# Optimization experiments

Measured on AMD Instinct MI355X. Metric: run time of the kernel, lower is better.

The kernel has to match this reference:

```python
import jax, jax.numpy as jnp
import numpy as np

D_MODEL = 1024
H = 4
DK = 128   # head_qk_dim (key_dim=512)
DV = 256   # head_v_dim (value_dim=1024)
EPS = 1e-5
SCALE = DK ** -0.5


def setup_inputs() -> dict:
    key = jax.random.key(0)
    ks = jax.random.split(key, 8)
    w = lambda k, i, o: jax.random.normal(k, (i, o), jnp.float32) * (2.0 ** -2.5) * (6.0 / (i + o)) ** 0.5 * 2
    return {
        "x": jax.random.normal(ks[0], (2, 4096, D_MODEL), jnp.float32),
        "Wq": w(ks[1], D_MODEL, H * DK),
        "Wk": w(ks[2], D_MODEL, H * DK),
        "Wv": w(ks[3], D_MODEL, H * DV),
        "Wb": w(ks[4], D_MODEL, H),
        "Wg": w(ks[5], D_MODEL, H * DV),
        "Wo": w(ks[6], H * DV, D_MODEL),
        "norm_w": jnp.ones((DV,), jnp.float32),
    }


def _delta_rule(q, k, v, beta):
    """Delta-rule linear attention. q,k: [b,n,h,dk], v: [b,n,h,dv], beta: [b,n,h].
    S_t = S_{t-1} + k_t (beta_t * (v_t - k_t^T S_{t-1}))^T ; o_t = q_t^T S_t."""
    b = q.shape[0]
    # time-major for scan: [n,b,h,*]
    qt = jnp.moveaxis(q, 1, 0)
    kt = jnp.moveaxis(k, 1, 0)
    vt = jnp.moveaxis(v, 1, 0)
    bt = jnp.moveaxis(beta, 1, 0)
    S0 = jnp.zeros((b, H, DK, DV), q.dtype)

    def step(S, inp):
        q_t, k_t, v_t, b_t = inp
        pred = jnp.einsum('bhk,bhkv->bhv', k_t, S)          # current memory readout
        delta = (v_t - pred) * b_t[..., None]                # beta-scaled error
        S = S + k_t[..., :, None] * delta[..., None, :]      # rank-1 update [b,h,dk,dv]
        o_t = jnp.einsum('bhk,bhkv->bhv', q_t, S)
        return S, o_t

    _, o = jax.lax.scan(step, S0, (qt, kt, vt, bt))          # o: [n,b,h,dv]
    return jnp.moveaxis(o, 0, 1)                             # [b,n,h,dv]


def reference(x, Wq, Wk, Wv, Wb, Wg, Wo, norm_w):
    b, n, _ = x.shape
    q = (x @ Wq).reshape(b, n, H, DK)
    k = (x @ Wk).reshape(b, n, H, DK)
    v = (x @ Wv).reshape(b, n, H, DV)
    beta = jax.nn.sigmoid(x @ Wb)                            # [b,n,h]
    # L2-normalize keys (delta-rule kernels assume unit-norm k) and scale q
    k = k * jax.lax.rsqrt(jnp.sum(k * k, axis=-1, keepdims=True) + 1e-12)
    q = q * SCALE
    o = _delta_rule(q, k, v, beta)                           # [b,n,h,dv]
    # FusedRMSNormSwishGate over head_v_dim
    g = (x @ Wg).reshape(b, n, H, DV)
    o = o * jax.lax.rsqrt(jnp.mean(o * o, axis=-1, keepdims=True) + EPS) * norm_w
    o = o * (g * jax.nn.sigmoid(g))                          # swish gate
    return o.reshape(b, n, H * DV) @ Wo
```

## Files before the change

kernel.cpp:

```cpp
#include <hip/hip_runtime.h>
#include <hip/hip_bf16.h>
#include <stdint.h>
#include <stddef.h>

typedef __attribute__((ext_vector_type(8))) short short8v;
typedef __attribute__((ext_vector_type(4))) float f32x4;
typedef unsigned short us;

__device__ __forceinline__ float bf2f(unsigned short u) {
    return __uint_as_float(((unsigned int)u) << 16);
}
__device__ __forceinline__ unsigned short f2bf(float f) {
    unsigned int x = __float_as_uint(f);
    x += 0x7fffu + ((x >> 16) & 1u);
    return (unsigned short)(x >> 16);
}
__device__ __forceinline__ unsigned int cvtpk(float lo, float hi) {
    unsigned int r;
    asm("v_cvt_pk_bf16_f32 %0, %1, %2" : "=v"(r) : "v"(lo), "v"(hi));
    return r;
}

#define NTOK 8192
#define DM   1024
#define NPROJ 3072
#define SEQ  4096
#define NCHUNK 64
#define SCQ 0.08838834764831845f

#define GLDS16(g, l) __builtin_amdgcn_global_load_lds( \
    (const __attribute__((address_space(1))) void*)(g), \
    (__attribute__((address_space(3))) void*)(l), 16, 0, 0)

__device__ __forceinline__ void bar_lgkm() {
    asm volatile("s_waitcnt lgkmcnt(0)" ::: "memory");
    __builtin_amdgcn_s_barrier();
    __builtin_amdgcn_sched_barrier(0);
}

__device__ __forceinline__ int sw16(int row, int k) {
    int u = k >> 3;
    int us_ = (u & 8) | ((u ^ row) & 7);
    return row * 128 + us_ * 8 + (k & 7);
}
__device__ __forceinline__ int sw8(int row, int k) {
    int u = k >> 3;
    int us_ = (u ^ row) & 7;
    return row * 64 + us_ * 8 + (k & 7);
}
__device__ __forceinline__ int sw128(int row, int k) {
    int u = k >> 3;
    return row * 128 + ((u ^ row) & 15) * 8 + (k & 7);
}
__device__ __forceinline__ int sw64(int row, int k) {
    int u = k >> 3;
    return row * 64 + ((u ^ row) & 7) * 8 + (k & 7);
}
__device__ __forceinline__ int sw64b(int row, int k) {
    int u = k >> 3;
    return row * 64 + ((u ^ row ^ (row >> 3)) & 7) * 8 + (k & 7);
}
__device__ __forceinline__ int swU(int t, int j) {
    int jj = j & 127, u = jj >> 3;
    int us_ = (u & 8) | ((u ^ t) & 7);
    return t * 256 + (j >> 7) * 128 + us_ * 8 + (jj & 7);
}

__global__ __launch_bounds__(256) void prep(
    const float* __restrict__ x, us* __restrict__ xb,
    const float* __restrict__ Wb, float* __restrict__ beta,
    const float* __restrict__ Wq, const float* __restrict__ Wk,
    const float* __restrict__ Wv, const float* __restrict__ Wg,
    const float* __restrict__ Wo, us* __restrict__ WT, us* __restrict__ WoT)
{
    __shared__ float smem[64 * 65];
    int tid = threadIdx.x;
    int bid = blockIdx.x;

    if (bid < 4096) {
        int i = bid * 256 + tid;
        int tok = i >> 7;
        int kb = (i >> 3) & 15;
        int u = i & 7;
        int ko = kb * 64 + ((u ^ (tok & 7)) * 8);
        const float4* src = (const float4*)(x + (size_t)tok * 1024 + ko);
        float4 v0 = src[0], v1 = src[1];
        uint4 o;
        o.x = cvtpk(v0.x, v0.y); o.y = cvtpk(v0.z, v0.w);
        o.z = cvtpk(v1.x, v1.y); o.w = cvtpk(v1.z, v1.w);
        *(uint4*)(xb + (size_t)i * 8) = o;
        const float4* wbv = (const float4*)Wb;
        float xs[8] = {v0.x, v0.y, v0.z, v0.w, v1.x, v1.y, v1.z, v1.w};
        float4 s = {0.f, 0.f, 0.f, 0.f};
        #pragma unroll
        for (int e = 0; e < 8; e++) {
            float4 w = wbv[ko + e];
            s.x += xs[e] * w.x; s.y += xs[e] * w.y;
            s.z += xs[e] * w.z; s.w += xs[e] * w.w;
        }
        *(float4*)&smem[tid * 4] = s;
        __syncthreads();
        if (tid < 8) {
            int tp = tid >> 2, h = tid & 3;
            float acc = 0.f;
            for (int j = 0; j < 128; j++) acc += smem[(tp * 128 + j) * 4 + h];
            beta[(size_t)(bid * 2 + tp) * 4 + h] = 1.f / (1.f + __expf(-acc));
        }
        return;
    }

    int lb = bid - 4096;
    const float* srcw; us* dst; int N;
    if (lb < 128)      { srcw = Wq; dst = WT;                    N = 512;  }
    else if (lb < 256) { srcw = Wk; dst = WT + (size_t)512 * DM;  N = 512;  lb -= 128; }
    else if (lb < 512) { srcw = Wv; dst = WT + (size_t)1024 * DM; N = 1024; lb -= 256; }
    else if (lb < 768) { srcw = Wg; dst = WT + (size_t)2048 * DM; N = 1024; lb -= 512; }
    else               { srcw = Wo; dst = WoT;                   N = 1024; lb -= 768; }
    int nbx = N >> 6;
    int n0 = (lb % nbx) * 64, k0 = (lb / nbx) * 64;
    float (*tl)[65] = (float(*)[65])smem;
    int tr = tid >> 6, tc = tid & 63;
    #pragma unroll
    for (int i2 = 0; i2 < 16; i2++) {
        int kk = 4 * i2 + tr;
        tl[kk][tc] = srcw[(size_t)(k0 + kk) * N + n0 + tc];
    }
    __syncthreads();
    int n = tid >> 2, seg = (tid & 3) * 16;
    short8v a, b;
    #pragma unroll
    for (int e = 0; e < 8; e++) {
        a[e] = (short)f2bf(tl[seg + e][n]);
        b[e] = (short)f2bf(tl[seg + 8 + e][n]);
    }
    int n_ = n0 + n;
    int o1 = (tid & 3) * 2, o2_ = o1 + 1;
    us* d = dst + (size_t)n_ * DM + k0;
    *(short8v*)(d + (o1 ^ (n_ & 7)) * 8) = a;
    *(short8v*)(d + (o2_ ^ (n_ & 7)) * 8) = b;
}

template<int OUT_F32>
__global__ __launch_bounds__(256) void gemm_bt(
    const us* __restrict__ A, const us* __restrict__ BT,
    void* __restrict__ C, int M, int N, int K)
{
    __shared__ us As[2][128 * 64];
    __shared__ us Bs[2][128 * 64];
    int tid = threadIdx.x;
    int wave = tid >> 6, lane = tid & 63;
    int wr = (wave >> 1) * 64, wc = (wave & 1) * 64;
    int fr = lane & 15, fq = lane >> 4;
    int nbx = gridDim.x, nwg = nbx * gridDim.y;
    int wg = blockIdx.y * nbx + blockIdx.x;
    int cpx = nwg >> 3;
    wg = (wg & 7) * cpx + (wg >> 3);
    int m0 = (wg % nbx) * 128, n0 = (wg / nbx) * 128;

    f32x4 acc[4][4];
    #pragma unroll
    for (int i = 0; i < 4; i++)
        #pragma unroll
        for (int j = 0; j < 4; j++) acc[i][j] = (f32x4){0.f, 0.f, 0.f, 0.f};

    int rl = lane >> 3, ul = lane & 7;

    auto issue = [&](int k0, int bufi) {
        #pragma unroll
        for (int i = 0; i < 4; i++) {
            int row = wave * 32 + i * 8 + rl;
            GLDS16(&A[(size_t)(m0 + row) * K + k0 + ul * 8], &As[bufi][(wave * 32 + i * 8) * 64]);
            GLDS16(&BT[(size_t)(n0 + row) * K + k0 + ul * 8], &Bs[bufi][(wave * 32 + i * 8) * 64]);
        }
    };

    int NT = K >> 6;
    issue(0, 0);
    if (NT > 1) issue(64, 1);

    for (int t = 0; t < NT; t++) {
        if (t + 1 < NT) asm volatile("s_waitcnt vmcnt(8)" ::: "memory");
        else            asm volatile("s_waitcnt vmcnt(0)" ::: "memory");
        __builtin_amdgcn_sched_barrier(0);
        __builtin_amdgcn_s_barrier();
        __builtin_amdgcn_sched_barrier(0);
        const us* as = As[t & 1];
        const us* bs = Bs[t & 1];
        #pragma unroll
        for (int kk = 0; kk < 2; kk++) {
            short8v a[4], b[4];
            #pragma unroll
            for (int i = 0; i < 4; i++) {
                int ra = wr + i * 16 + fr;
                a[i] = *(const short8v*)&as[ra * 64 + ((4 * kk + fq) ^ (ra & 7)) * 8];
                int rb = wc + i * 16 + fr;
                b[i] = *(const short8v*)&bs[rb * 64 + ((4 * kk + fq) ^ (rb & 7)) * 8];
            }
            #pragma unroll
            for (int i = 0; i < 4; i++)
                #pragma unroll
                for (int j = 0; j < 4; j++)
                    acc[i][j] = __builtin_amdgcn_mfma_f32_16x16x32_bf16(a[i], b[j], acc[i][j], 0, 0, 0);
        }
        bar_lgkm();
        if (t + 2 < NT) issue((t + 2) * 64, t & 1);
    }

    #pragma unroll
    for (int i = 0; i < 4; i++)
        #pragma unroll
        for (int j = 0; j < 4; j++)
            #pragma unroll
            for (int t = 0; t < 4; t++) {
                int row = m0 + wr + i * 16 + fq * 4 + t;
                int col = n0 + wc + j * 16 + fr;
                float val = acc[i][j][t];
                if (OUT_F32) ((float*)C)[(size_t)row * N + col] = val;
                else ((us*)C)[(size_t)row * N + col] = f2bf(val);
            }
}

__global__ __launch_bounds__(256) void chunk_pre(
    const us* __restrict__ QKVG, const float* __restrict__ beta,
    us* __restrict__ Wbuf, us* __restrict__ Ubuf,
    us* __restrict__ Kbuf, us* __restrict__ KTbuf)
{
    __shared__ us Ks[8192];
    __shared__ us KTs[8192];
    __shared__ us VT[8192];
    __shared__ us Tb[4096];
    __shared__ float Af[64][64];
    __shared__ float betas[64];

    int c = blockIdx.x, bh = blockIdx.y;
    int b = bh >> 2, h = bh & 3;
    int tid = threadIdx.x;
    int wv = tid >> 6, ln = tid & 63;
    int fr = ln & 15, fq = ln >> 4;
    int tok0 = b * SEQ + c * 64;
    size_t cb = (size_t)bh * NCHUNK + c;

    #pragma unroll
    for (int r = 0; r < 4; r++) {
        int idx = tid + 256 * r;
        int t = idx >> 4, u = idx & 15;
        short8v kv = *(const short8v*)(QKVG + (size_t)(tok0 + t) * NPROJ + 512 + h * 128 + u * 8);
        *(short8v*)(Ks + sw16(t, u * 8)) = kv;
    }
    if (tid < 64) betas[tid] = beta[(size_t)(tok0 + tid) * 4 + h];
    __syncthreads();

    {
        int t = tid >> 2, p = tid & 3;
        short8v v[4];
        float ss = 0.f;
        #pragma unroll
        for (int uu = 0; uu < 4; uu++) {
            v[uu] = *(const short8v*)(Ks + sw16(t, (p * 4 + uu) * 8));
            #pragma unroll
            for (int e = 0; e < 8; e++) {
                float f = bf2f((unsigned short)v[uu][e]);
                ss += f * f;
            }
        }
        ss += __shfl_xor(ss, 1);
        ss += __shfl_xor(ss, 2);
        float rn = rsqrtf(ss + 1e-12f);
        #pragma unroll
        for (int uu = 0; uu < 4; uu++) {
            short8v o;
            #pragma unroll
            for (int e = 0; e < 8; e++)
                o[e] = (short)f2bf(bf2f((unsigned short)v[uu][e]) * rn);
            *(short8v*)(Ks + sw16(t, (p * 4 + uu) * 8)) = o;
        }
    }
    __syncthreads();

    {
        f32x4 aacc[4];
        #pragma unroll
        for (int jt = 0; jt < 4; jt++) aacc[jt] = (f32x4){0.f, 0.f, 0.f, 0.f};
        #pragma unroll
        for (int ks = 0; ks < 4; ks++) {
            short8v ak = *(const short8v*)(Ks + sw16(16 * wv + fr, 32 * ks + 8 * fq));
            #pragma unroll
            for (int jt = 0; jt < 4; jt++) {
                short8v bk = *(const short8v*)(Ks + sw16(16 * jt + fr, 32 * ks + 8 * fq));
                aacc[jt] = __builtin_amdgcn_mfma_f32_16x16x32_bf16(ak, bk, aacc[jt], 0, 0, 0);
            }
        }
        #pragma unroll
        for (int jt = 0; jt < 4; jt++)
            #pragma unroll
            for (int r = 0; r < 4; r++) {
                int t = 16 * wv + 4 * fq + r, s = 16 * jt + fr;
                if (s < t) Af[t][s] = betas[t] * aacc[jt][r];
            }
    }
    __syncthreads();

    if (wv == 0) {
        int cc = ln;
        for (int tb = 0; tb < 8; tb++) {
            int base = tb * 8;
            float xs[8];
            #pragma unroll
            for (int i = 0; i < 8; i++) {
                int t = base + i;
                float v = Af[t][cc];
                #pragma unroll
                for (int s = 0; s < i; s++)
                    v += Af[t][base + s] * xs[s];
                float xt = (cc < t) ? -v : 0.f;
                xs[i] = xt;
                if (cc < t) Af[t][cc] = xt;
            }
            for (int r = base + 8; r < 64; r += 2) {
                float u0 = 0.f, u1 = 0.f;
                #pragma unroll
                for (int s = 0; s < 8; s++) {
                    float a0 = Af[r][base + s];
                    float a1 = Af[r + 1][base + s];
                    u0 += a0 * xs[s];
                    u1 += a1 * xs[s];
                }
                Af[r][cc] += u0;
                Af[r + 1][cc] += u1;
            }
        }
    } else {
        int q = tid - 64;
        for (int g = q; g < 1024; g += 192) {
            int t = g >> 4, u = g & 15;
            short8v kv = *(const short8v*)(Ks + sw16(t, u * 8));
            #pragma unroll
            for (int e = 0; e < 8; e++)
                KTs[sw64b(u * 8 + e, t)] = (unsigned short)kv[e];
        }
        for (int g = q; g < 1024; g += 192) {
            int t = g >> 4, jg = g & 15;
            short8v vv = *(const short8v*)(QKVG + (size_t)(tok0 + t) * NPROJ + 1024 + h * 256 + jg * 8);
            #pragma unroll
            for (int e = 0; e < 8; e++)
                VT[sw64b(jg * 8 + e, t)] = (unsigned short)vv[e];
        }
    }
    __syncthreads();

    {
        #pragma unroll
        for (int i = 0; i < 4; i++) {
            int idx = tid + 256 * i;
            int t = idx >> 4, u = idx & 15;
            short8v kv = *(const short8v*)(Ks + sw16(t, u * 8));
            *(short8v*)(Kbuf + cb * 8192 + t * 128 + (size_t)(((u ^ t) & 15) * 8)) = kv;
        }
        #pragma unroll
        for (int i = 0; i < 16; i++) {
            int idx = tid + 256 * i;
            int t = idx >> 6, s = idx & 63;
            float tv = (s < t) ? Af[t][s] : (s == t ? 1.f : 0.f);
            Tb[sw8(t, s)] = f2bf(tv * betas[s]);
        }
        #pragma unroll
        for (int i = 0; i < 4; i++) {
            int idx = tid + 256 * i;
            *(short8v*)(KTbuf + cb * 8192 + (size_t)idx * 8) =
                *(const short8v*)(KTs + (size_t)idx * 8);
        }
    }
    __syncthreads();

    {
        f32x4 wacc[8], uacc[8];
        #pragma unroll
        for (int jt = 0; jt < 8; jt++) {
            wacc[jt] = (f32x4){0.f, 0.f, 0.f, 0.f};
            uacc[jt] = (f32x4){0.f, 0.f, 0.f, 0.f};
        }
        #pragma unroll
        for (int ks = 0; ks < 2; ks++) {
            short8v at = *(const short8v*)(Tb + sw8(16 * wv + fr, 32 * ks + 8 * fq));
            #pragma unroll
            for (int jt = 0; jt < 8; jt++) {
                short8v bk = *(const short8v*)(KTs + sw64b(16 * jt + fr, 32 * ks + 8 * fq));
                wacc[jt] = __builtin_amdgcn_mfma_f32_16x16x32_bf16(at, bk, wacc[jt], 0, 0, 0);
                short8v bv = *(const short8v*)(VT + sw64b(16 * jt + fr, 32 * ks + 8 * fq));
                uacc[jt] = __builtin_amdgcn_mfma_f32_16x16x32_bf16(at, bv, uacc[jt], 0, 0, 0);
            }
        }
        #pragma unroll
        for (int jt = 0; jt < 8; jt++)
            #pragma unroll
            for (int r = 0; r < 4; r++) {
                int t = 16 * wv + 4 * fq + r, d = 16 * jt + fr;
                Wbuf[cb * 8192 + (d >> 6) * 4096 + sw64(t, d & 63)] = f2bf(-wacc[jt][r]);
                Ubuf[cb * 16384 + swU(t, d)] = f2bf(uacc[jt][r]);
            }
    }
    __syncthreads();

    #pragma unroll
    for (int i = 0; i < 4; i++) {
        int g = tid + 256 * i;
        int t = g >> 4, jg = g & 15;
        short8v vv = *(const short8v*)(QKVG + (size_t)(tok0 + t) * NPROJ + 1024 + h * 256 + 128 + jg * 8);
        #pragma unroll
        for (int e = 0; e < 8; e++)
            VT[sw64b(jg * 8 + e, t)] = (unsigned short)vv[e];
    }
    __syncthreads();
    {
        f32x4 uacc[8];
        #pragma unroll
        for (int jt = 0; jt < 8; jt++) uacc[jt] = (f32x4){0.f, 0.f, 0.f, 0.f};
        #pragma unroll
        for (int ks = 0; ks < 2; ks++) {
            short8v at = *(const short8v*)(Tb + sw8(16 * wv + fr, 32 * ks + 8 * fq));
            #pragma unroll
            for (int jt = 0; jt < 8; jt++) {
                short8v bv = *(const short8v*)(VT + sw64b(16 * jt + fr, 32 * ks + 8 * fq));
                uacc[jt] = __builtin_amdgcn_mfma_f32_16x16x32_bf16(at, bv, uacc[jt], 0, 0, 0);
            }
        }
        #pragma unroll
        for (int jt = 0; jt < 8; jt++)
            #pragma unroll
            for (int r = 0; r < 4; r++) {
                int t = 16 * wv + 4 * fq + r, j = 16 * jt + fr;
                Ubuf[cb * 16384 + swU(t, 128 + j)] = f2bf(uacc[jt][r]);
            }
    }
}

#define SCW 0
#define SCKT 8192
#define SCU 16384
#define SCBUF 17408
#define SSTB (2 * SCBUF)
#define SDTB (2 * SCBUF + 2048)

__global__ __launch_bounds__(256, 1) void fused_scan_qg(
    const us* __restrict__ xb, const us* __restrict__ WT, us* __restrict__ QKVG,
    const us* __restrict__ Wbuf, const us* __restrict__ Ubuf,
    const us* __restrict__ KTbuf, us* __restrict__ Sbuf)
{
    extern __shared__ us lds[];
    int tid = threadIdx.x;

    if (blockIdx.x < 128) {
        if (tid >= 128) {
            for (int c = 0; c < NCHUNK; c++) __builtin_amdgcn_s_barrier();
            return;
        }
        int wv = tid >> 6, ln = tid & 63;
        int fr = ln & 15, fq = ln >> 4;
        int sl = blockIdx.x >> 3;
        int j0 = sl * 16;
        int bh = blockIdx.x & 7;

        short8v id0;
        #pragma unroll
        for (int e = 0; e < 8; e++)
            id0[e] = (short)((8 * fq + e == fr) ? 0x3F80 : 0);

        f32x4 sacc[4];
        #pragma unroll
        for (int i = 0; i < 4; i++) sacc[i] = (f32x4){0.f, 0.f, 0.f, 0.f};

        us* ST = lds + SSTB + wv * 1024;

        auto issue = [&](int c1) {
            size_t cb = (size_t)bh * NCHUNK + c1;
            us* dst = lds + (c1 & 1) * SCBUF;
            const us* Wc = Wbuf + cb * 8192 + wv * 4096;
            const us* Kc = KTbuf + cb * 8192 + wv * 4096;
            #pragma unroll
            for (int i = 0; i < 8; i++) {
                GLDS16(Wc + i * 512 + ln * 8, dst + SCW + wv * 4096 + i * 512);
                GLDS16(Kc + i * 512 + ln * 8, dst + SCKT + wv * 4096 + i * 512);
            }
            if (wv) {
                const us* Uc = Ubuf + cb * 16384;
                #pragma unroll
                for (int i = 0; i < 2; i++) {
                    int t = i * 32 + (ln >> 1);
                    GLDS16(Uc + swU(t, j0 + (ln & 1) * 8), dst + SCU + i * 512);
                }
            }
        };

        issue(0);

        for (int c = 0; c < NCHUNK; c++) {
            const us* ba = lds + (c & 1) * SCBUF;
            us* DTw = lds + SDTB + (c & 1) * 2048 + wv * 1024;
            const us* DTr = lds + SDTB + (c & 1) * 2048;
            size_t sb = ((size_t)bh * NCHUNK + c) * 32768 + sl * 2048 + wv * 1024;

            #pragma unroll
            for (int dt = 0; dt < 4; dt++) {
                uint2 w;
                w.x = cvtpk(sacc[dt][0], sacc[dt][1]);
                w.y = cvtpk(sacc[dt][2], sacc[dt][3]);
                int dl = 16 * dt + 4 * fq;
                int off = fr * 64 + (((dl >> 3) ^ fr) & 7) * 8 + (dl & 7);
                *(uint2*)&ST[off] = w;
                *(uint2*)(Sbuf + sb + off) = w;
            }
            if (c + 1 < NCHUNK) issue(c + 1);
            if (c + 1 < NCHUNK) {
                if (wv) asm volatile("s_waitcnt vmcnt(22)" ::: "memory");
                else    asm volatile("s_waitcnt vmcnt(20)" ::: "memory");
            } else {
                asm volatile("s_waitcnt vmcnt(4)" ::: "memory");
            }
            __builtin_amdgcn_sched_barrier(0);

            f32x4 dacc[4];
            #pragma unroll
            for (int tt = 0; tt < 4; tt++) dacc[tt] = (f32x4){0.f, 0.f, 0.f, 0.f};
            #pragma unroll
            for (int kc = 0; kc < 2; kc++) {
                short8v bs = *(const short8v*)&ST[fr * 64 + (((4 * kc + fq) ^ fr) & 7) * 8];
                #pragma unroll
                for (int tt = 0; tt < 4; tt++) {
                    short8v aw = *(const short8v*)&ba[SCW + wv * 4096 + sw64(16 * tt + fr, 32 * kc + 8 * fq)];
                    dacc[tt] = __builtin_amdgcn_mfma_f32_16x16x32_bf16(aw, bs, dacc[tt], 0, 0, 0);
                }
            }
            if (wv) {
                #pragma unroll
                for (int tt = 0; tt < 4; tt++) {
                    short8v au = *(const short8v*)&ba[SCU + (16 * tt + fr) * 16 + 8 * (fq & 1)];
                    dacc[tt] = __builtin_amdgcn_mfma_f32_16x16x32_bf16(au, id0, dacc[tt], 0, 0, 0);
                }
            }
            #pragma unroll
            for (int tt = 0; tt < 4; tt++) {
                uint2 w;
                w.x = cvtpk(dacc[tt][0], dacc[tt][1]);
                w.y = cvtpk(dacc[tt][2], dacc[tt][3]);
                int tl = 16 * tt + 4 * fq;
                *(uint2*)&DTw[fr * 64 + (((tl >> 3) ^ fr) & 7) * 8 + (tl & 7)] = w;
            }
            bar_lgkm();
            #pragma unroll
            for (int kc2 = 0; kc2 < 2; kc2++) {
                int o = fr * 64 + (((4 * kc2 + fq) ^ fr) & 7) * 8;
                short8v bd0 = *(const short8v*)&DTr[o];
                short8v bd1 = *(const short8v*)&DTr[1024 + o];
                #pragma unroll
                for (int dt = 0; dt < 4; dt++) {
                    short8v ak = *(const short8v*)&ba[SCKT + sw64b(64 * wv + 16 * dt + fr, 32 * kc2 + 8 * fq)];
                    sacc[dt] = __builtin_amdgcn_mfma_f32_16x16x32_bf16(ak, bd0, sacc[dt], 0, 0, 0);
                    sacc[dt] = __builtin_amdgcn_mfma_f32_16x16x32_bf16(ak, bd1, sacc[dt], 0, 0, 0);
                }
            }
        }
        return;
    }

    {
        us* As = lds;
        us* Bs = lds + 8192;
        int wave = tid >> 6, lane = tid & 63;
        int wr = (wave >> 1) * 64, wc = (wave & 1) * 64;
        int fr = lane & 15, fq = lane >> 4;
        int wg = blockIdx.x - 128;
        wg = (wg & 7) * 96 + (wg >> 3);
        int m0 = (wg % 64) * 128;
        int ntile = wg / 64;
        int n0 = ntile * 128 + (ntile >= 4 ? 1536 : 0);

        f32x4 acc[4][4];
        #pragma unroll
        for (int i = 0; i < 4; i++)
            #pragma unroll
            for (int j = 0; j < 4; j++) acc[i][j] = (f32x4){0.f, 0.f, 0.f, 0.f};

        int rl = lane >> 3, ul = lane & 7;

        for (int k0 = 0; k0 < DM; k0 += 64) {
            #pragma unroll
            for (int i = 0; i < 4; i++) {
                int row = wave * 32 + i * 8 + rl;
                GLDS16(&xb[(size_t)(m0 + row) * DM + k0 + ul * 8], As + (wave * 32 + i * 8) * 64);
                GLDS16(&WT[(size_t)(n0 + row) * DM + k0 + ul * 8], Bs + (wave * 32 + i * 8) * 64);
            }
            __syncthreads();
            #pragma unroll
            for (int kk = 0; kk < 2; kk++) {
                short8v a[4], b[4];
                #pragma unroll
                for (int i = 0; i < 4; i++) {
                    int ra = wr + i * 16 + fr;
                    a[i] = *(const short8v*)&As[ra * 64 + ((4 * kk + fq) ^ (ra & 7)) * 8];
                    int rb = wc + i * 16 + fr;
                    b[i] = *(const short8v*)&Bs[rb * 64 + ((4 * kk + fq) ^ (rb & 7)) * 8];
                }
                #pragma unroll
                for (int i = 0; i < 4; i++)
                    #pragma unroll
                    for (int j = 0; j < 4; j++)
                        acc[i][j] = __builtin_amdgcn_mfma_f32_16x16x32_bf16(a[i], b[j], acc[i][j], 0, 0, 0);
            }
            __syncthreads();
        }
        #pragma unroll
        for (int i = 0; i < 4; i++)
            #pragma unroll
            for (int j = 0; j < 4; j++)
                #pragma unroll
                for (int t = 0; t < 4; t++) {
                    int row = m0 + wr + i * 16 + fq * 4 + t;
                    int col = n0 + wc + j * 16 + fr;
                    QKVG[(size_t)row * NPROJ + col] = f2bf(acc[i][j][t]);
                }
    }
}

#define OKW 0
#define OKK 8192
#define OKP 16384
#define OKS 20480
#define OKDT 53248

__global__ __launch_bounds__(512, 1) void out_k(
    const us* __restrict__ QKVG, const us* __restrict__ Wbuf,
    const us* __restrict__ Ubuf, const us* __restrict__ Kbuf,
    const us* __restrict__ Sbuf, const float* __restrict__ norm_w,
    us* __restrict__ o2)
{
    extern __shared__ us lds[];
    int tid = threadIdx.x;
    int wvg = (tid >> 6) & 3;
    int jh = tid >> 8;
    int ln = tid & 63;
    int fr = ln & 15, fq = ln >> 4;
    int c = blockIdx.x;
    int bh = blockIdx.y;
    int b = bh >> 2, h = bh & 3;
    int tok0 = b * SEQ + c * 64;
    size_t cb = (size_t)bh * NCHUNK + c;

    short8v id0, id1;
    #pragma unroll
    for (int e = 0; e < 8; e++) {
        id0[e] = (short)((8 * fq + e == fr) ? 0x3F80 : 0);
        id1[e] = (short)((8 * fq + e == fr + 16) ? 0x3F80 : 0);
    }

    #pragma unroll
    for (int i = 0; i < 2; i++) {
        int q = (tid + 512 * i) * 8;
        GLDS16(Wbuf + cb * 8192 + q, lds + OKW + q);
        GLDS16(Kbuf + cb * 8192 + q, lds + OKK + q);
    }
    #pragma unroll
    for (int i = 0; i < 8; i++) {
        int q = (tid + 512 * i) * 8;
        GLDS16(Sbuf + cb * 32768 + q, lds + OKS + q);
    }
    short8v qf[4];
    #pragma unroll
    for (int ks = 0; ks < 4; ks++)
        qf[ks] = *(const short8v*)(QKVG + (size_t)(tok0 + 16 * wvg + fr) * NPROJ
                                   + h * 128 + ks * 32 + fq * 8);
    __syncthreads();

    f32x4 dacc[8], oacc[8];
    #pragma unroll
    for (int jt = 0; jt < 8; jt++) {
        dacc[jt] = (f32x4){0.f, 0.f, 0.f, 0.f};
        oacc[jt] = (f32x4){0.f, 0.f, 0.f, 0.f};
    }
    #pragma unroll
    for (int ks = 0; ks < 4; ks++) {
        short8v aw = *(const short8v*)&lds[OKW + (ks >> 1) * 4096
            + sw64(16 * wvg + fr, (ks & 1) * 32 + 8 * fq)];
        short8v aq = qf[ks];
        #pragma unroll
        for (int jt = 0; jt < 8; jt++) {
            short8v bs = *(const short8v*)&lds[OKS + jh * 16384 + jt * 2048 + (ks >> 1) * 1024
                + fr * 64 + ((((ks & 1) * 4 + fq) ^ fr) & 7) * 8];
            dacc[jt] = __builtin_amdgcn_mfma_f32_16x16x32_bf16(aw, bs, dacc[jt], 0, 0, 0);
            oacc[jt] = __builtin_amdgcn_mfma_f32_16x16x32_bf16(aq, bs, oacc[jt], 0, 0, 0);
        }
    }
    #pragma unroll
    for (int ju = 0; ju < 4; ju++) {
        short8v au = *(const short8v*)(Ubuf + cb * 16384
            + swU(16 * wvg + fr, jh * 128 + 32 * ju + 8 * fq));
        dacc[2 * ju + 0] = __builtin_amdgcn_mfma_f32_16x16x32_bf16(au, id0, dacc[2 * ju + 0], 0, 0, 0);
        dacc[2 * ju + 1] = __builtin_amdgcn_mfma_f32_16x16x32_bf16(au, id1, dacc[2 * ju + 1], 0, 0, 0);
    }
    if (jh == 0) {
        f32x4 pacc[4];
        #pragma unroll
        for (int jt2 = 0; jt2 < 4; jt2++) pacc[jt2] = (f32x4){0.f, 0.f, 0.f, 0.f};
        #pragma unroll
        for (int ks = 0; ks < 4; ks++) {
            short8v aq = qf[ks];
            #pragma unroll
            for (int jt2 = 0; jt2 < 4; jt2++) {
                short8v bk = *(const short8v*)&lds[OKK + sw128(16 * jt2 + fr, 32 * ks + 8 * fq)];
                pacc[jt2] = __builtin_amdgcn_mfma_f32_16x16x32_bf16(aq, bk, pacc[jt2], 0, 0, 0);
            }
        }
        #pragma unroll
        for (int jt2 = 0; jt2 < 4; jt2++)
            #pragma unroll
            for (int r = 0; r < 4; r++) {
                int t = 16 * wvg + 4 * fq + r, s = 16 * jt2 + fr;
                float val = (s <= t) ? pacc[jt2][r] * SCQ : 0.f;
                lds[OKP + sw64(t, s)] = f2bf(val);
            }
    }
    #pragma unroll
    for (int jt = 0; jt < 8; jt++)
        #pragma unroll
        for (int r = 0; r < 4; r++) oacc[jt][r] *= SCQ;
    #pragma unroll
    for (int jt = 0; jt < 8; jt++) {
        int jg = jh * 128 + 16 * jt + fr;
        int t0 = 16 * wvg + 4 * fq;
        uint2 w;
        w.x = cvtpk(dacc[jt][0], dacc[jt][1]);
        w.y = cvtpk(dacc[jt][2], dacc[jt][3]);
        *(uint2*)&lds[OKDT + sw64(jg, t0)] = w;
    }
    bar_lgkm();

    #pragma unroll
    for (int ks = 0; ks < 2; ks++) {
        short8v ap = *(const short8v*)&lds[OKP + sw64(16 * wvg + fr, 32 * ks + 8 * fq)];
        #pragma unroll
        for (int jt = 0; jt < 8; jt++) {
            short8v bd = *(const short8v*)&lds[OKDT + sw64(jh * 128 + 16 * jt + fr, 32 * ks + 8 * fq)];
            oacc[jt] = __builtin_amdgcn_mfma_f32_16x16x32_bf16(ap, bd, oacc[jt], 0, 0, 0);
        }
    }
    __syncthreads();

    float* OSf = (float*)lds;
    #pragma unroll
    for (int jt = 0; jt < 8; jt++)
        #pragma unroll
        for (int r = 0; r < 4; r++) {
            int t = 16 * wvg + 4 * fq + r;
            OSf[t * 260 + jh * 128 + 16 * jt + fr] = oacc[jt][r];
        }
    #pragma unroll
    for (int l = 0; l < 4; l++) {
        int idx = tid + 512 * l;
        int tt = idx >> 5, ccol = (idx & 31) * 8;
        GLDS16(QKVG + (size_t)(tok0 + tt) * NPROJ + 2048 + h * 256 + ccol,
               lds + OKDT + idx * 8);
    }
    __syncthreads();

    {
        int t = tid >> 3, p = tid & 7;
        int tok = tok0 + t;
        f32x4 ov[8];
        float ssum = 0.f;
        #pragma unroll
        for (int g = 0; g < 8; g++) {
            ov[g] = *(const f32x4*)&OSf[t * 260 + 32 * p + 4 * g];
            ssum += ov[g][0] * ov[g][0] + ov[g][1] * ov[g][1]
                  + ov[g][2] * ov[g][2] + ov[g][3] * ov[g][3];
        }
        ssum += __shfl_xor(ssum, 1);
        ssum += __shfl_xor(ssum, 2);
        ssum += __shfl_xor(ssum, 4);
        float rr = rsqrtf(ssum * (1.0f / 256.0f) + 1e-5f);
        #pragma unroll
        for (int g = 0; g < 8; g++) {
            int j0g = 32 * p + 4 * g;
            uint2 gv = *(const uint2*)&lds[OKDT + t * 256 + j0g];
            float4 nw = *(const float4*)&norm_w[j0g];
            float g0 = bf2f((us)gv.x), g1 = bf2f((us)(gv.x >> 16));
            float g2 = bf2f((us)gv.y), g3 = bf2f((us)(gv.y >> 16));
            float r0 = ov[g][0] * rr * nw.x * (g0 / (1.f + __expf(-g0)));
            float r1 = ov[g][1] * rr * nw.y * (g1 / (1.f + __expf(-g1)));
            float r2 = ov[g][2] * rr * nw.z * (g2 / (1.f + __expf(-g2)));
            float r3 = ov[g][3] * rr * nw.w * (g3 / (1.f + __expf(-g3)));
            uint2 w;
            w.x = cvtpk(r0, r1);
            w.y = cvtpk(r2, r3);
            int u = h * 32 + (j0g >> 3);
            size_t dsto = (size_t)tok * 1024 + (size_t)(u >> 3) * 64
                        + (size_t)(((u & 7) ^ (tok & 7)) * 8) + (j0g & 7);
            *(uint2*)&o2[dsto] = w;
        }
    }
}

extern "C" void kernel_launch(void* const* d_in, const int* in_sizes, int n_in,
                              void* d_out, int out_size, void* d_ws, size_t ws_size,
                              hipStream_t stream) {
    const float* x      = (const float*)d_in[0];
    const float* Wq     = (const float*)d_in[1];
    const float* Wk     = (const float*)d_in[2];
    const float* Wv     = (const float*)d_in[3];
    const float* Wb     = (const float*)d_in[4];
    const float* Wg     = (const float*)d_in[5];
    const float* Wo     = (const float*)d_in[6];
    const float* norm_w = (const float*)d_in[7];
    float* out = (float*)d_out;

    char* ws = (char*)d_ws;
    us*    xb   = (us*)(ws + 0);
    us*    o2   = (us*)(ws + 0);
    us*    WT   = (us*)(ws + 16777216);
    us*    KTbuf= (us*)(ws + 23068672);
    us*    QKVG = (us*)(ws + 31457280);
    float* beta = (float*)(ws + 81788928);
    us*    Wbuf = (us*)(ws + 81920000);
    us*    Ubuf = (us*)(ws + 90308608);
    us*    Kbuf = (us*)(ws + 107085824);
    us*    WoT  = (us*)(ws + 115474432);
    us*    Sbuf = (us*)(ws + 117571584);

    (void)hipFuncSetAttribute((const void*)fused_scan_qg,
                              hipFuncAttributeMaxDynamicSharedMemorySize, 81920);
    (void)hipFuncSetAttribute((const void*)out_k,
                              hipFuncAttributeMaxDynamicSharedMemorySize, 139264);

    prep<<<5120, 256, 0, stream>>>(x, xb, Wb, beta, Wq, Wk, Wv, Wg, Wo, WT, WoT);
    gemm_bt<0><<<dim3(64, 12), 256, 0, stream>>>(xb, WT + (size_t)512 * DM,
                                                 (void*)(QKVG + 512), NTOK, NPROJ, DM);
    chunk_pre<<<dim3(NCHUNK, 8), 256, 0, stream>>>(QKVG, beta, Wbuf, Ubuf, Kbuf, KTbuf);
    fused_scan_qg<<<896, 256, 81920, stream>>>(xb, WT, QKVG, Wbuf, Ubuf, KTbuf, Sbuf);
    out_k<<<dim3(NCHUNK, 8), 512, 139264, stream>>>(QKVG, Wbuf, Ubuf, Kbuf, Sbuf, norm_w, o2);
    gemm_bt<1><<<dim3(64, 8), 256, 0, stream>>>(o2, WoT, (void*)out, NTOK, DM, DM);
}
```

Before: 229.2 us.

## Pack two scan slices per block to share W and K chunk loads

The scan part of the fused kernel now uses 64 blocks instead of 128. Each block runs two independent column slices, one per pair of waves, where previously two waves idled. The W and K^T chunk tiles are loaded once into LDS and shared by both slices, and the load work is split across all four waves. This halves global traffic for the shared tiles and frees CUs for the concurrent GEMM blocks. The cost is more LDS per block (96KB), an extra block barrier per chunk, and retuned vmcnt waits.

New measurement: 229.4 us. Within noise of the previous version (+0.1%).

```diff
diff --git a/kernel.cpp b/kernel.cpp
--- a/kernel.cpp
+++ b/kernel.cpp
@@ -434,12 +434,11 @@
     }
 }
 
-#define SCW 0
-#define SCKT 8192
-#define SCU 16384
-#define SCBUF 17408
-#define SSTB (2 * SCBUF)
-#define SDTB (2 * SCBUF + 2048)
+#define Z2W(p)    ((p) * 8192)
+#define Z2KT(p)   (16384 + (p) * 8192)
+#define Z2U(p, u) (32768 + (p) * 2048 + (u) * 1024)
+#define Z2ST(u)   (36864 + (u) * 2048)
+#define Z2DT(p, u) (40960 + (p) * 4096 + (u) * 2048)
 
 __global__ __launch_bounds__(256, 1) void fused_scan_qg(
     const us* __restrict__ xb, const us* __restrict__ WT, us* __restrict__ QKVG,
@@ -449,16 +448,15 @@
     extern __shared__ us lds[];
     int tid = threadIdx.x;
 
-    if (blockIdx.x < 128) {
-        if (tid >= 128) {
-            for (int c = 0; c < NCHUNK; c++) __builtin_amdgcn_s_barrier();
-            return;
-        }
-        int wv = tid >> 6, ln = tid & 63;
+    if (blockIdx.x < 64) {
+        int gw = tid >> 6;
+        int un = tid >> 7;
+        int wv = gw & 1;
+        int ln = tid & 63;
         int fr = ln & 15, fq = ln >> 4;
-        int sl = blockIdx.x >> 3;
-        int j0 = sl * 16;
         int bh = blockIdx.x & 7;
+        int slp = blockIdx.x >> 3;
+        int sl = slp * 2 + un;
 
         short8v id0;
         #pragma unroll
@@ -469,34 +467,37 @@
         #pragma unroll
         for (int i = 0; i < 4; i++) sacc[i] = (f32x4){0.f, 0.f, 0.f, 0.f};
 
-        us* ST = lds + SSTB + wv * 1024;
-
         auto issue = [&](int c1) {
             size_t cb = (size_t)bh * NCHUNK + c1;
-            us* dst = lds + (c1 & 1) * SCBUF;
-            const us* Wc = Wbuf + cb * 8192 + wv * 4096;
-            const us* Kc = KTbuf + cb * 8192 + wv * 4096;
-            #pragma unroll
-            for (int i = 0; i < 8; i++) {
-                GLDS16(Wc + i * 512 + ln * 8, dst + SCW + wv * 4096 + i * 512);
-                GLDS16(Kc + i * 512 + ln * 8, dst + SCKT + wv * 4096 + i * 512);
-            }
-            if (wv) {
+            int p = c1 & 1;
+            if (gw < 2) {
+                const us* Wc = Wbuf + cb * 8192 + gw * 4096;
+                #pragma unroll
+                for (int i = 0; i < 8; i++)
+                    GLDS16(Wc + i * 512 + ln * 8, lds + Z2W(p) + gw * 4096 + i * 512);
                 const us* Uc = Ubuf + cb * 16384;
+                int j0s = slp * 32 + gw * 16;
                 #pragma unroll
                 for (int i = 0; i < 2; i++) {
                     int t = i * 32 + (ln >> 1);
-                    GLDS16(Uc + swU(t, j0 + (ln & 1) * 8), dst + SCU + i * 512);
+                    GLDS16(Uc + swU(t, j0s + (ln & 1) * 8), lds + Z2U(p, gw) + i * 512);
                 }
+            } else {
+                int hf = gw & 1;
+                const us* Kc = KTbuf + cb * 8192 + hf * 4096;
+                #pragma unroll
+                for (int i = 0; i < 8; i++)
+                    GLDS16(Kc + i * 512 + ln * 8, lds + Z2KT(p) + hf * 4096 + i * 512);
             }
         };
 
         issue(0);
 
         for (int c = 0; c < NCHUNK; c++) {
-            const us* ba = lds + (c & 1) * SCBUF;
-            us* DTw = lds + SDTB + (c & 1) * 2048 + wv * 1024;
-            const us* DTr = lds + SDTB + (c & 1) * 2048;
+            int p = c & 1;
+            us* ST = lds + Z2ST(un) + wv * 1024;
+            us* DTw = lds + Z2DT(p, un) + wv * 1024;
+            const us* DTr = lds + Z2DT(p, un);
             size_t sb = ((size_t)bh * NCHUNK + c) * 32768 + sl * 2048 + wv * 1024;
 
             #pragma unroll
@@ -511,12 +512,13 @@
             }
             if (c + 1 < NCHUNK) issue(c + 1);
             if (c + 1 < NCHUNK) {
-                if (wv) asm volatile("s_waitcnt vmcnt(22)" ::: "memory");
-                else    asm volatile("s_waitcnt vmcnt(20)" ::: "memory");
+                if (gw < 2) asm volatile("s_waitcnt vmcnt(14)" ::: "memory");
+                else        asm volatile("s_waitcnt vmcnt(12)" ::: "memory");
             } else {
                 asm volatile("s_waitcnt vmcnt(4)" ::: "memory");
             }
             __builtin_amdgcn_sched_barrier(0);
+            bar_lgkm();
 
             f32x4 dacc[4];
             #pragma unroll
@@ -526,14 +528,15 @@
                 short8v bs = *(const short8v*)&ST[fr * 64 + (((4 * kc + fq) ^ fr) & 7) * 8];
                 #pragma unroll
                 for (int tt = 0; tt < 4; tt++) {
-                    short8v aw = *(const short8v*)&ba[SCW + wv * 4096 + sw64(16 * tt + fr, 32 * kc + 8 * fq)];
+                    short8v aw = *(const short8v*)&lds[Z2W(p) + wv * 4096
+                        + sw64(16 * tt + fr, 32 * kc + 8 * fq)];
                     dacc[tt] = __builtin_amdgcn_mfma_f32_16x16x32_bf16(aw, bs, dacc[tt], 0, 0, 0);
                 }
             }
             if (wv) {
                 #pragma unroll
                 for (int tt = 0; tt < 4; tt++) {
-                    short8v au = *(const short8v*)&ba[SCU + (16 * tt + fr) * 16 + 8 * (fq & 1)];
+                    short8v au = *(const short8v*)&lds[Z2U(p, un) + (16 * tt + fr) * 16 + 8 * (fq & 1)];
                     dacc[tt] = __builtin_amdgcn_mfma_f32_16x16x32_bf16(au, id0, dacc[tt], 0, 0, 0);
                 }
             }
@@ -553,7 +556,8 @@
                 short8v bd1 = *(const short8v*)&DTr[1024 + o];
                 #pragma unroll
                 for (int dt = 0; dt < 4; dt++) {
-                    short8v ak = *(const short8v*)&ba[SCKT + sw64b(64 * wv + 16 * dt + fr, 32 * kc2 + 8 * fq)];
+                    short8v ak = *(const short8v*)&lds[Z2KT(p)
+                        + sw64b(64 * wv + 16 * dt + fr, 32 * kc2 + 8 * fq)];
                     sacc[dt] = __builtin_amdgcn_mfma_f32_16x16x32_bf16(ak, bd0, sacc[dt], 0, 0, 0);
                     sacc[dt] = __builtin_amdgcn_mfma_f32_16x16x32_bf16(ak, bd1, sacc[dt], 0, 0, 0);
                 }
@@ -568,7 +572,7 @@
         int wave = tid >> 6, lane = tid & 63;
         int wr = (wave >> 1) * 64, wc = (wave & 1) * 64;
         int fr = lane & 15, fq = lane >> 4;
-        int wg = blockIdx.x - 128;
+        int wg = blockIdx.x - 64;
         wg = (wg & 7) * 96 + (wg >> 3);
         int m0 = (wg % 64) * 128;
         int ntile = wg / 64;
@@ -825,7 +829,7 @@
     us*    Sbuf = (us*)(ws + 117571584);
 
     (void)hipFuncSetAttribute((const void*)fused_scan_qg,
-                              hipFuncAttributeMaxDynamicSharedMemorySize, 81920);
+                              hipFuncAttributeMaxDynamicSharedMemorySize, 98304);
     (void)hipFuncSetAttribute((const void*)out_k,
                               hipFuncAttributeMaxDynamicSharedMemorySize, 139264);
 
@@ -833,7 +837,7 @@
     gemm_bt<0><<<dim3(64, 12), 256, 0, stream>>>(xb, WT + (size_t)512 * DM,
                                                  (void*)(QKVG + 512), NTOK, NPROJ, DM);
     chunk_pre<<<dim3(NCHUNK, 8), 256, 0, stream>>>(QKVG, beta, Wbuf, Ubuf, Kbuf, KTbuf);
-    fused_scan_qg<<<896, 256, 81920, stream>>>(xb, WT, QKVG, Wbuf, Ubuf, KTbuf, Sbuf);
+    fused_scan_qg<<<832, 256, 98304, stream>>>(xb, WT, QKVG, Wbuf, Ubuf, KTbuf, Sbuf);
     out_k<<<dim3(NCHUNK, 8), 512, 139264, stream>>>(QKVG, Wbuf, Ubuf, Kbuf, Sbuf, norm_w, o2);
     gemm_bt<1><<<dim3(64, 8), 256, 0, stream>>>(o2, WoT, (void*)out, NTOK, DM, DM);
 }
```
